# Performance work log

Hardware: AMD Instinct MI355X
Metric: run time of the kernel (lower is better)

The kernel has to match this reference:

```python
import jax, jax.numpy as jnp
import numpy as np

N_ATOMS = 50000
N_EDGES = 800000
NODE_DIM = 64
EDGE_DIM = 64
FULL_DIM = 2 * NODE_DIM + EDGE_DIM
BN_EPS = 1e-5


def setup_inputs() -> dict:
    key = jax.random.key(0)
    ks = jax.random.split(key, 8)
    atom_features = jax.random.normal(ks[0], (N_ATOMS, NODE_DIM), dtype=jnp.float32)
    edge_features = jax.random.normal(ks[1], (N_EDGES, EDGE_DIM), dtype=jnp.float32)
    edge_indices = jax.random.randint(ks[2], (N_EDGES, 2), 0, N_ATOMS, dtype=jnp.int64)
    lim = 1.0 / np.sqrt(FULL_DIM)
    W_filter = jax.random.uniform(ks[3], (NODE_DIM, FULL_DIM), jnp.float32, -lim, lim)
    b_filter = jax.random.uniform(ks[4], (NODE_DIM,), jnp.float32, -lim, lim)
    W_core = jax.random.uniform(ks[5], (NODE_DIM, FULL_DIM), jnp.float32, -lim, lim)
    b_core = jax.random.uniform(ks[6], (NODE_DIM,), jnp.float32, -lim, lim)
    gamma_filter = jnp.ones((NODE_DIM,), jnp.float32)
    beta_filter = jnp.zeros((NODE_DIM,), jnp.float32)
    gamma_core = jnp.ones((NODE_DIM,), jnp.float32)
    beta_core = jnp.zeros((NODE_DIM,), jnp.float32)
    return {
        "atom_features": atom_features,
        "edge_features": edge_features,
        "W_filter": W_filter, "b_filter": b_filter,
        "gamma_filter": gamma_filter, "beta_filter": beta_filter,
        "W_core": W_core, "b_core": b_core,
        "gamma_core": gamma_core, "beta_core": beta_core,
        "edge_indices": edge_indices,
    }


def _batchnorm(x, gamma, beta):
    # training-mode BN over the edge axis (biased variance, as torch uses for normalization)
    mean = jnp.mean(x, axis=0)
    var = jnp.mean(jnp.square(x - mean), axis=0)
    return (x - mean) * jax.lax.rsqrt(var + BN_EPS) * gamma + beta


def reference(atom_features, edge_features, W_filter, b_filter, gamma_filter,
              beta_filter, W_core, b_core, gamma_core, beta_core, edge_indices):
    src = edge_indices[:, 0]
    dst = edge_indices[:, 1]
    # z_ij: [E, 2*node_dim + edge_dim]
    z = jnp.concatenate([atom_features[dst], atom_features[src], edge_features], axis=1)
    signal = jax.nn.softplus(_batchnorm(z @ W_core.T + b_core, gamma_core, beta_core))
    gate = jax.nn.sigmoid(_batchnorm(z @ W_filter.T + b_filter, gamma_filter, beta_filter))
    message = gate * signal  # [E, node_dim]
    nbr_sumed = jax.ops.segment_sum(message, dst, num_segments=atom_features.shape[0])
    return atom_features + nbr_sumed
```

## Files before the change

### kernel.cpp

```cpp
#include <hip/hip_runtime.h>
#include <hip/hip_bf16.h>
#include <math.h>

#define N_ATOMS   50000
#define N_EDGES   800000
#define KDIM      192
#define BN_EPS    1e-5f

#define TILE_E     64
#define TPB        5
#define NTILES     (N_EDGES / TILE_E)
#define GRID1      (NTILES / TPB)
#define STAT_SLOTS 32
#define ZSTRIDE    200
#define NSCANBLK   ((N_ATOMS + 255) / 256)

typedef __attribute__((ext_vector_type(8))) __bf16 bf16x8;
typedef __attribute__((ext_vector_type(4))) float  f32x4;
typedef __attribute__((ext_vector_type(4))) unsigned short u16x4;

__device__ __forceinline__ ushort f2bf(float f) {
    union { float f; unsigned u; } v; v.f = f;
    unsigned u = v.u;
    return (ushort)((u + 0x7FFFu + ((u >> 16) & 1u)) >> 16);
}
__device__ __forceinline__ float bf2f(unsigned hi16) {
    union { unsigned u; float f; } v; v.u = hi16 << 16; return v.f;
}
__device__ __forceinline__ float msgf(unsigned pv, float sc_c, float sh_c,
                                      float sc_f, float sh_f) {
    float pc = fmaf(bf2f(pv & 0xFFFFu), sc_c, sh_c);
    float pf = fmaf(bf2f(pv >> 16),     sc_f, sh_f);
    float sp = fmaxf(pc, 0.f) + __logf(1.f + __expf(-fabsf(pc)));
    float sg = 1.f / (1.f + __expf(-pf));
    return sp * sg;
}

__device__ __forceinline__ void gather_issue(
    const float* __restrict__ atom, const float* __restrict__ edgef,
    const int* __restrict__ eidx, int tilebase, int tid, f32x4* v)
{
    const int er = tid >> 4, f4 = tid & 15;
#pragma unroll
    for (int it = 0; it < 12; ++it) {
        const int seg = it >> 2;
        const int e   = (it & 3) * 16 + er;
        const float* srcp;
        if (seg == 0)      srcp = atom  + (size_t)eidx[2 * (tilebase + e) + 1] * 64;
        else if (seg == 1) srcp = atom  + (size_t)eidx[2 * (tilebase + e)] * 64;
        else               srcp = edgef + (size_t)(tilebase + e) * 64;
        v[it] = *(const f32x4*)(srcp + f4 * 4);
    }
}

__device__ __forceinline__ void gather_commit(const f32x4* v, ushort* zl, int tid)
{
    const int er = tid >> 4, f4 = tid & 15;
#pragma unroll
    for (int it = 0; it < 12; ++it) {
        const int seg = it >> 2;
        const int e   = (it & 3) * 16 + er;
        u16x4 b;
        b.x = f2bf(v[it].x); b.y = f2bf(v[it].y);
        b.z = f2bf(v[it].z); b.w = f2bf(v[it].w);
        *(u16x4*)&zl[e * ZSTRIDE + seg * 64 + f4 * 4] = b;
    }
}

__global__ __launch_bounds__(256) void gemm_stats_store(
    const float* __restrict__ atom, const float* __restrict__ edgef,
    const ushort* __restrict__ Wb, const int* __restrict__ eidx,
    const unsigned* __restrict__ row_start, const unsigned* __restrict__ rank,
    float* __restrict__ stat_partial, unsigned* __restrict__ ws_pre,
    int do_store)
{
    __shared__ __align__(16) ushort zbuf[2][TILE_E * ZSTRIDE];
    __shared__ unsigned perml[TPB * TILE_E];
    const int tid  = threadIdx.x;
    const int lane = tid & 63, wave = tid >> 6;
    const int ch = wave >> 1, rp = wave & 1;
    const int row = lane & 15, quad = lane >> 4;

    const int t0 = blockIdx.x * TPB;
    if (do_store) {
        for (int i = tid; i < TPB * TILE_E; i += 256) {
            const int e = t0 * TILE_E + i;
            const int d = eidx[2 * e + 1];
            perml[i] = row_start[d] + rank[e];
        }
    }

    bf16x8 bfr[2][2][6];
#pragma unroll
    for (int m = 0; m < 2; ++m)
#pragma unroll
        for (int nt = 0; nt < 2; ++nt)
#pragma unroll
            for (int ks = 0; ks < 6; ++ks)
                bfr[m][nt][ks] = *(const bf16x8*)&Wb[
                    (size_t)(m * 64 + ch * 32 + nt * 16 + row) * KDIM + ks * 32 + quad * 8];

    float s[2][2] = {{0.f, 0.f}, {0.f, 0.f}};
    float q[2][2] = {{0.f, 0.f}, {0.f, 0.f}};

    f32x4 pre[12];
    gather_issue(atom, edgef, eidx, t0 * TILE_E, tid, pre);

    for (int tt = 0; tt < TPB; ++tt) {
        ushort* zl = zbuf[tt & 1];
        gather_commit(pre, zl, tid);
        __syncthreads();
        if (tt + 1 < TPB)
            gather_issue(atom, edgef, eidx, (t0 + tt + 1) * TILE_E, tid, pre);

#pragma unroll
        for (int ett = 0; ett < 2; ++ett) {
            const ushort* zb = zl + ((2 * rp + ett) * 16 + row) * ZSTRIDE;
            bf16x8 a[6];
#pragma unroll
            for (int ks = 0; ks < 6; ++ks)
                a[ks] = *(const bf16x8*)&zb[ks * 32 + quad * 8];
            f32x4 acc[2][2];
#pragma unroll
            for (int m = 0; m < 2; ++m)
#pragma unroll
                for (int nt = 0; nt < 2; ++nt)
                    acc[m][nt] = (f32x4){0.f, 0.f, 0.f, 0.f};
#pragma unroll
            for (int ks = 0; ks < 6; ++ks)
#pragma unroll
                for (int m = 0; m < 2; ++m)
#pragma unroll
                    for (int nt = 0; nt < 2; ++nt)
                        acc[m][nt] = __builtin_amdgcn_mfma_f32_16x16x32_bf16(
                            a[ks], bfr[m][nt][ks], acc[m][nt], 0, 0, 0);
#pragma unroll
            for (int nt = 0; nt < 2; ++nt) {
                const int c = ch * 32 + nt * 16 + row;
#pragma unroll
                for (int r = 0; r < 4; ++r) {
                    float vc = acc[0][nt][r], vf = acc[1][nt][r];
                    s[0][nt] += vc; q[0][nt] += vc * vc;
                    s[1][nt] += vf; q[1][nt] += vf * vf;
                    if (do_store) {
                        const int eloc = (2 * rp + ett) * 16 + quad * 4 + r;
                        const unsigned pos = perml[tt * TILE_E + eloc];
                        unsigned pack = (unsigned)f2bf(vc) | ((unsigned)f2bf(vf) << 16);
                        ws_pre[(size_t)pos * 64 + c] = pack;
                    }
                }
            }
        }
    }

    float* slot = stat_partial + (size_t)(blockIdx.x & (STAT_SLOTS - 1)) * 256;
#pragma unroll
    for (int m = 0; m < 2; ++m)
#pragma unroll
        for (int nt = 0; nt < 2; ++nt) {
            float sv = s[m][nt], qv = q[m][nt];
            sv += __shfl_xor(sv, 16, 64); sv += __shfl_xor(sv, 32, 64);
            qv += __shfl_xor(qv, 16, 64); qv += __shfl_xor(qv, 32, 64);
            if (lane < 16) {
                int c = ch * 32 + nt * 16 + lane;
                atomicAdd(slot + m * 128 + c, sv);
                atomicAdd(slot + m * 128 + 64 + c, qv);
            }
        }
}

__global__ __launch_bounds__(256) void setup_all(
    const float* __restrict__ Wc, const float* __restrict__ Wf,
    ushort* __restrict__ Wb, float* __restrict__ stat_partial,
    unsigned* __restrict__ counts)
{
    int i = blockIdx.x * 256 + threadIdx.x;
    if (i < 2 * 64 * KDIM) {
        float v = (i < 64 * KDIM) ? Wc[i] : Wf[i - 64 * KDIM];
        Wb[i] = f2bf(v);
    }
    if (i < STAT_SLOTS * 256) stat_partial[i] = 0.f;
    if (i < N_ATOMS) counts[i] = 0u;
}

__global__ void finalize_stats(const float* __restrict__ stat_partial,
                               const float* __restrict__ gc, const float* __restrict__ btc,
                               const float* __restrict__ gf, const float* __restrict__ btf,
                               float* __restrict__ params)
{
    int t = threadIdx.x;
    bool isf = t >= 64;
    int j = t & 63;
    float s = 0.f, q = 0.f;
    for (int slot = 0; slot < STAT_SLOTS; slot++) {
        const float* sp = stat_partial + (size_t)slot * 256 + (isf ? 128 : 0);
        s += sp[j];
        q += sp[64 + j];
    }
    float mean = s / (float)N_EDGES;
    float var  = q / (float)N_EDGES - mean * mean;
    float inv  = rsqrtf(var + BN_EPS);
    float gamma = isf ? gf[j] : gc[j];
    float beta  = isf ? btf[j] : btc[j];
    float scale = gamma * inv;
    float shift = beta - mean * scale;
    params[t]       = scale;
    params[128 + t] = shift;
}

__global__ __launch_bounds__(256) void hist_rank(const int* __restrict__ eidx,
                                                 unsigned* __restrict__ counts,
                                                 unsigned* __restrict__ rank)
{
    int e = blockIdx.x * 256 + threadIdx.x;
    rank[e] = atomicAdd(&counts[eidx[2 * e + 1]], 1u);
}

__global__ __launch_bounds__(256) void scan_a(const unsigned* __restrict__ counts,
                                              unsigned* __restrict__ row_start,
                                              unsigned* __restrict__ blksum)
{
    __shared__ unsigned sh[256];
    const int tid = threadIdx.x;
    const int i = blockIdx.x * 256 + tid;
    unsigned v = (i < N_ATOMS) ? counts[i] : 0u;
    sh[tid] = v;
    __syncthreads();
    for (int off = 1; off < 256; off <<= 1) {
        unsigned t = (tid >= off) ? sh[tid - off] : 0u;
        __syncthreads();
        sh[tid] += t;
        __syncthreads();
    }
    if (i < N_ATOMS) row_start[i] = sh[tid] - v;
    if (tid == 255) blksum[blockIdx.x] = sh[tid];
}

__global__ void scan_b(unsigned* __restrict__ blksum)
{
    __shared__ unsigned sh[256];
    const int tid = threadIdx.x;
    unsigned v = (tid < NSCANBLK) ? blksum[tid] : 0u;
    sh[tid] = v;
    __syncthreads();
    for (int off = 1; off < 256; off <<= 1) {
        unsigned t = (tid >= off) ? sh[tid - off] : 0u;
        __syncthreads();
        sh[tid] += t;
        __syncthreads();
    }
    if (tid < NSCANBLK) blksum[tid] = sh[tid] - v;
}

__global__ __launch_bounds__(256) void init_row(unsigned* __restrict__ row_start,
                                                const unsigned* __restrict__ blksum)
{
    int i = blockIdx.x * 256 + threadIdx.x;
    if (i < N_ATOMS) row_start[i] += blksum[i >> 8];
    if (i == 0) row_start[N_ATOMS] = N_EDGES;
}

__global__ __launch_bounds__(256) void bn_act_reduce(
    const unsigned* __restrict__ ws_pre, const unsigned* __restrict__ row_start,
    const float* __restrict__ atom, const float* __restrict__ params,
    float* __restrict__ out)
{
    const int lane = threadIdx.x & 63;
    const int a    = blockIdx.x * 4 + (threadIdx.x >> 6);

    const float sc_c = params[lane],      sh_c = params[128 + lane];
    const float sc_f = params[64 + lane], sh_f = params[192 + lane];

    const unsigned jb = row_start[a];
    const unsigned n  = row_start[a + 1] - jb;
    const unsigned* base = ws_pre + (size_t)jb * 64 + lane;

    float acc = 0.f;
    unsigned k = 0;
    for (; k + 8 <= n; k += 8) {
        unsigned p[8];
#pragma unroll
        for (int u = 0; u < 8; ++u) p[u] = base[(size_t)(k + u) * 64];
#pragma unroll
        for (int u = 0; u < 8; ++u) acc += msgf(p[u], sc_c, sh_c, sc_f, sh_f);
    }
    for (; k < n; ++k) acc += msgf(base[(size_t)k * 64], sc_c, sh_c, sc_f, sh_f);

    out[(size_t)a * 64 + lane] = atom[(size_t)a * 64 + lane] + acc;
}

__global__ __launch_bounds__(256) void copy_out(const f32x4* __restrict__ src,
                                                f32x4* __restrict__ dst)
{
    int i = blockIdx.x * blockDim.x + threadIdx.x;
    dst[i] = src[i];
}

__global__ __launch_bounds__(256) void apply_scatter_fb(
    const float* __restrict__ atom, const float* __restrict__ edgef,
    const ushort* __restrict__ Wb, const int* __restrict__ eidx,
    const float* __restrict__ params, float* __restrict__ out)
{
    __shared__ __align__(16) ushort zl[TILE_E * ZSTRIDE];
    const int tid  = threadIdx.x;
    const int lane = tid & 63, wave = tid >> 6;
    const int ch = wave >> 1, rp = wave & 1;
    const int row = lane & 15, quad = lane >> 4;

    bf16x8 bfr[2][2][6];
#pragma unroll
    for (int m = 0; m < 2; ++m)
#pragma unroll
        for (int nt = 0; nt < 2; ++nt)
#pragma unroll
            for (int ks = 0; ks < 6; ++ks)
                bfr[m][nt][ks] = *(const bf16x8*)&Wb[
                    (size_t)(m * 64 + ch * 32 + nt * 16 + row) * KDIM + ks * 32 + quad * 8];

    float scc[2], shc[2], scf[2], shf[2];
#pragma unroll
    for (int nt = 0; nt < 2; ++nt) {
        int c = ch * 32 + nt * 16 + row;
        scc[nt] = params[c];        shc[nt] = params[128 + c];
        scf[nt] = params[64 + c];   shf[nt] = params[192 + c];
    }

    const int t0 = blockIdx.x * TPB;
    for (int tt = 0; tt < TPB; ++tt) {
        const int tilebase = (t0 + tt) * TILE_E;
        f32x4 pre[12];
        gather_issue(atom, edgef, eidx, tilebase, tid, pre);
        __syncthreads();
        gather_commit(pre, zl, tid);
        __syncthreads();
#pragma unroll
        for (int ett = 0; ett < 2; ++ett) {
            const ushort* zb = zl + ((2 * rp + ett) * 16 + row) * ZSTRIDE;
            bf16x8 a[6];
#pragma unroll
            for (int ks = 0; ks < 6; ++ks)
                a[ks] = *(const bf16x8*)&zb[ks * 32 + quad * 8];
            f32x4 acc[2][2];
#pragma unroll
            for (int m = 0; m < 2; ++m)
#pragma unroll
                for (int nt = 0; nt < 2; ++nt)
                    acc[m][nt] = (f32x4){0.f, 0.f, 0.f, 0.f};
#pragma unroll
            for (int ks = 0; ks < 6; ++ks)
#pragma unroll
                for (int m = 0; m < 2; ++m)
#pragma unroll
                    for (int nt = 0; nt < 2; ++nt)
                        acc[m][nt] = __builtin_amdgcn_mfma_f32_16x16x32_bf16(
                            a[ks], bfr[m][nt][ks], acc[m][nt], 0, 0, 0);
#pragma unroll
            for (int nt = 0; nt < 2; ++nt) {
                int c = ch * 32 + nt * 16 + row;
#pragma unroll
                for (int r = 0; r < 4; ++r) {
                    float pc = fmaf(acc[0][nt][r], scc[nt], shc[nt]);
                    float pf = fmaf(acc[1][nt][r], scf[nt], shf[nt]);
                    float sp = fmaxf(pc, 0.f) + __logf(1.f + __expf(-fabsf(pc)));
                    float sg = 1.f / (1.f + __expf(-pf));
                    int eloc = (2 * rp + ett) * 16 + quad * 4 + r;
                    int d = eidx[2 * (tilebase + eloc) + 1];
                    atomicAdd(out + (size_t)d * 64 + c, sp * sg);
                }
            }
        }
    }
}

extern "C" void kernel_launch(void* const* d_in, const int* in_sizes, int n_in,
                              void* d_out, int out_size, void* d_ws, size_t ws_size,
                              hipStream_t stream)
{
    const float* atom  = (const float*)d_in[0];
    const float* edgef = (const float*)d_in[1];
    const float* Wf    = (const float*)d_in[2];
    const float* gf    = (const float*)d_in[4];
    const float* btf   = (const float*)d_in[5];
    const float* Wc    = (const float*)d_in[6];
    const float* gc    = (const float*)d_in[8];
    const float* btc   = (const float*)d_in[9];
    const int*   eidx  = (const int*)d_in[10];
    float* out = (float*)d_out;

    unsigned* ws_pre       = (unsigned*)d_ws;
    float*    stat_partial = (float*)(ws_pre + (size_t)N_EDGES * 64);
    float*    params       = stat_partial + STAT_SLOTS * 256;
    ushort*   Wb           = (ushort*)(params + 256);
    unsigned* counts       = (unsigned*)(Wb + 2 * 64 * KDIM);
    unsigned* row_start    = counts + N_ATOMS;
    unsigned* blksum       = row_start + N_ATOMS + 1;
    unsigned* rank         = blksum + 256;

    const size_t need_full = (size_t)((char*)(rank + N_EDGES) - (char*)d_ws);
    const int full = (ws_size >= need_full) ? 1 : 0;

    setup_all<<<256, 256, 0, stream>>>(Wc, Wf, Wb, stat_partial, counts);

    if (full) {
        hist_rank<<<N_EDGES / 256, 256, 0, stream>>>(eidx, counts, rank);
        scan_a<<<NSCANBLK, 256, 0, stream>>>(counts, row_start, blksum);
        scan_b<<<1, 256, 0, stream>>>(blksum);
        init_row<<<NSCANBLK, 256, 0, stream>>>(row_start, blksum);
        gemm_stats_store<<<GRID1, 256, 0, stream>>>(atom, edgef, Wb, eidx,
                                                    row_start, rank,
                                                    stat_partial, ws_pre, 1);
        finalize_stats<<<1, 128, 0, stream>>>(stat_partial, gc, btc, gf, btf, params);
        bn_act_reduce<<<N_ATOMS / 4, 256, 0, stream>>>(ws_pre, row_start,
                                                       atom, params, out);
    } else {
        gemm_stats_store<<<GRID1, 256, 0, stream>>>(atom, edgef, Wb, eidx,
                                                    (unsigned*)counts ,
                                                    (unsigned*)counts ,
                                                    stat_partial, ws_pre, 0);
        finalize_stats<<<1, 128, 0, stream>>>(stat_partial, gc, btc, gf, btf, params);
        copy_out<<<(N_ATOMS * 64 / 4) / 256, 256, 0, stream>>>(
            (const f32x4*)atom, (f32x4*)out);
        apply_scatter_fb<<<GRID1, 256, 0, stream>>>(atom, edgef, Wb, eidx,
                                                    params, out);
    }
}
```

Before: 493.7 us.

## Pre-convert atom features to bf16 for gathers and double tiles per block

Measured after the change: 482.1 us. -2.3%, faster.

```diff
diff --git a/kernel.cpp b/kernel.cpp
--- a/kernel.cpp
+++ b/kernel.cpp
@@ -8,7 +8,7 @@
 #define BN_EPS    1e-5f
 
 #define TILE_E     64
-#define TPB        5
+#define TPB        10
 #define NTILES     (N_EDGES / TILE_E)
 #define GRID1      (NTILES / TPB)
 #define STAT_SLOTS 32
@@ -34,6 +34,47 @@
     float sp = fmaxf(pc, 0.f) + __logf(1.f + __expf(-fabsf(pc)));
     float sg = 1.f / (1.f + __expf(-pf));
     return sp * sg;
+}
+
+__device__ __forceinline__ void gather_issue_m(
+    const ushort* __restrict__ atom_bf, const float* __restrict__ edgef,
+    const int* __restrict__ eidx, int tilebase, int tid,
+    u16x4* va, f32x4* ve)
+{
+    const int er = tid >> 4, f4 = tid & 15;
+#pragma unroll
+    for (int it = 0; it < 8; ++it) {
+        const int seg = it >> 2;
+        const int e   = (it & 3) * 16 + er;
+        const ushort* srcp =
+            atom_bf + (size_t)eidx[2 * (tilebase + e) + (seg == 0 ? 1 : 0)] * 64;
+        va[it] = *(const u16x4*)(srcp + f4 * 4);
+    }
+#pragma unroll
+    for (int it = 0; it < 4; ++it) {
+        const int e = it * 16 + er;
+        ve[it] = *(const f32x4*)(edgef + (size_t)(tilebase + e) * 64 + f4 * 4);
+    }
+}
+
+__device__ __forceinline__ void gather_commit_m(
+    const u16x4* va, const f32x4* ve, ushort* zl, int tid)
+{
+    const int er = tid >> 4, f4 = tid & 15;
+#pragma unroll
+    for (int it = 0; it < 8; ++it) {
+        const int seg = it >> 2;
+        const int e   = (it & 3) * 16 + er;
+        *(u16x4*)&zl[e * ZSTRIDE + seg * 64 + f4 * 4] = va[it];
+    }
+#pragma unroll
+    for (int it = 0; it < 4; ++it) {
+        const int e = it * 16 + er;
+        u16x4 b;
+        b.x = f2bf(ve[it].x); b.y = f2bf(ve[it].y);
+        b.z = f2bf(ve[it].z); b.w = f2bf(ve[it].w);
+        *(u16x4*)&zl[e * ZSTRIDE + 128 + f4 * 4] = b;
+    }
 }
 
 __device__ __forceinline__ void gather_issue(
@@ -68,7 +109,7 @@
 }
 
 __global__ __launch_bounds__(256) void gemm_stats_store(
-    const float* __restrict__ atom, const float* __restrict__ edgef,
+    const ushort* __restrict__ atom_bf, const float* __restrict__ edgef,
     const ushort* __restrict__ Wb, const int* __restrict__ eidx,
     const unsigned* __restrict__ row_start, const unsigned* __restrict__ rank,
     float* __restrict__ stat_partial, unsigned* __restrict__ ws_pre,
@@ -103,15 +144,17 @@
     float s[2][2] = {{0.f, 0.f}, {0.f, 0.f}};
     float q[2][2] = {{0.f, 0.f}, {0.f, 0.f}};
 
-    f32x4 pre[12];
-    gather_issue(atom, edgef, eidx, t0 * TILE_E, tid, pre);
+    u16x4 pva[8];
+    f32x4 pve[4];
+    gather_issue_m(atom_bf, edgef, eidx, t0 * TILE_E, tid, pva, pve);
 
     for (int tt = 0; tt < TPB; ++tt) {
         ushort* zl = zbuf[tt & 1];
-        gather_commit(pre, zl, tid);
+        gather_commit_m(pva, pve, zl, tid);
         __syncthreads();
         if (tt + 1 < TPB)
-            gather_issue(atom, edgef, eidx, (t0 + tt + 1) * TILE_E, tid, pre);
+            gather_issue_m(atom_bf, edgef, eidx, (t0 + tt + 1) * TILE_E, tid,
+                           pva, pve);
 
 #pragma unroll
         for (int ett = 0; ett < 2; ++ett) {
@@ -171,8 +214,9 @@
 
 __global__ __launch_bounds__(256) void setup_all(
     const float* __restrict__ Wc, const float* __restrict__ Wf,
-    ushort* __restrict__ Wb, float* __restrict__ stat_partial,
-    unsigned* __restrict__ counts)
+    const float* __restrict__ atom,
+    ushort* __restrict__ Wb, ushort* __restrict__ atom_bf,
+    float* __restrict__ stat_partial, unsigned* __restrict__ counts)
 {
     int i = blockIdx.x * 256 + threadIdx.x;
     if (i < 2 * 64 * KDIM) {
@@ -181,6 +225,12 @@
     }
     if (i < STAT_SLOTS * 256) stat_partial[i] = 0.f;
     if (i < N_ATOMS) counts[i] = 0u;
+    for (int j = i; j < N_ATOMS * 64 / 4; j += 256 * 256) {
+        f32x4 v = ((const f32x4*)atom)[j];
+        u16x4 b;
+        b.x = f2bf(v.x); b.y = f2bf(v.y); b.z = f2bf(v.z); b.w = f2bf(v.w);
+        ((u16x4*)atom_bf)[j] = b;
+    }
 }
 
 __global__ void finalize_stats(const float* __restrict__ stat_partial,
@@ -213,7 +263,8 @@
                                                  unsigned* __restrict__ rank)
 {
     int e = blockIdx.x * 256 + threadIdx.x;
-    rank[e] = atomicAdd(&counts[eidx[2 * e + 1]], 1u);
+    int2 p = ((const int2*)eidx)[e];
+    rank[e] = atomicAdd(&counts[p.y], 1u);
 }
 
 __global__ __launch_bounds__(256) void scan_a(const unsigned* __restrict__ counts,
@@ -296,10 +347,23 @@
     dst[i] = src[i];
 }
 
-__global__ __launch_bounds__(256) void apply_scatter_fb(
+__global__ __launch_bounds__(256) void convert_weights_fb(
+    const float* __restrict__ Wc, const float* __restrict__ Wf,
+    ushort* __restrict__ Wb, float* __restrict__ stat_partial)
+{
+    int i = blockIdx.x * 256 + threadIdx.x;
+    if (i < 2 * 64 * KDIM) {
+        float v = (i < 64 * KDIM) ? Wc[i] : Wf[i - 64 * KDIM];
+        Wb[i] = f2bf(v);
+    }
+    if (i < STAT_SLOTS * 256) stat_partial[i] = 0.f;
+}
+
+#define TPB_FB 5
+__global__ __launch_bounds__(256) void gemm_stats_fb(
     const float* __restrict__ atom, const float* __restrict__ edgef,
     const ushort* __restrict__ Wb, const int* __restrict__ eidx,
-    const float* __restrict__ params, float* __restrict__ out)
+    float* __restrict__ stat_partial)
 {
     __shared__ __align__(16) ushort zl[TILE_E * ZSTRIDE];
     const int tid  = threadIdx.x;
@@ -317,6 +381,87 @@
                 bfr[m][nt][ks] = *(const bf16x8*)&Wb[
                     (size_t)(m * 64 + ch * 32 + nt * 16 + row) * KDIM + ks * 32 + quad * 8];
 
+    float s[2][2] = {{0.f, 0.f}, {0.f, 0.f}};
+    float q[2][2] = {{0.f, 0.f}, {0.f, 0.f}};
+
+    const int t0 = blockIdx.x * TPB_FB;
+    for (int tt = 0; tt < TPB_FB; ++tt) {
+        const int tilebase = (t0 + tt) * TILE_E;
+        f32x4 pre[12];
+        gather_issue(atom, edgef, eidx, tilebase, tid, pre);
+        __syncthreads();
+        gather_commit(pre, zl, tid);
+        __syncthreads();
+#pragma unroll
+        for (int ett = 0; ett < 2; ++ett) {
+            const ushort* zb = zl + ((2 * rp + ett) * 16 + row) * ZSTRIDE;
+            bf16x8 a[6];
+#pragma unroll
+            for (int ks = 0; ks < 6; ++ks)
+                a[ks] = *(const bf16x8*)&zb[ks * 32 + quad * 8];
+            f32x4 acc[2][2];
+#pragma unroll
+            for (int m = 0; m < 2; ++m)
+#pragma unroll
+                for (int nt = 0; nt < 2; ++nt)
+                    acc[m][nt] = (f32x4){0.f, 0.f, 0.f, 0.f};
+#pragma unroll
+            for (int ks = 0; ks < 6; ++ks)
+#pragma unroll
+                for (int m = 0; m < 2; ++m)
+#pragma unroll
+                    for (int nt = 0; nt < 2; ++nt)
+                        acc[m][nt] = __builtin_amdgcn_mfma_f32_16x16x32_bf16(
+                            a[ks], bfr[m][nt][ks], acc[m][nt], 0, 0, 0);
+#pragma unroll
+            for (int nt = 0; nt < 2; ++nt) {
+#pragma unroll
+                for (int r = 0; r < 4; ++r) {
+                    float vc = acc[0][nt][r], vf = acc[1][nt][r];
+                    s[0][nt] += vc; q[0][nt] += vc * vc;
+                    s[1][nt] += vf; q[1][nt] += vf * vf;
+                }
+            }
+        }
+    }
+
+    float* slot = stat_partial + (size_t)(blockIdx.x & (STAT_SLOTS - 1)) * 256;
+#pragma unroll
+    for (int m = 0; m < 2; ++m)
+#pragma unroll
+        for (int nt = 0; nt < 2; ++nt) {
+            float sv = s[m][nt], qv = q[m][nt];
+            sv += __shfl_xor(sv, 16, 64); sv += __shfl_xor(sv, 32, 64);
+            qv += __shfl_xor(qv, 16, 64); qv += __shfl_xor(qv, 32, 64);
+            if (lane < 16) {
+                int c = ch * 32 + nt * 16 + lane;
+                atomicAdd(slot + m * 128 + c, sv);
+                atomicAdd(slot + m * 128 + 64 + c, qv);
+            }
+        }
+}
+
+__global__ __launch_bounds__(256) void apply_scatter_fb(
+    const float* __restrict__ atom, const float* __restrict__ edgef,
+    const ushort* __restrict__ Wb, const int* __restrict__ eidx,
+    const float* __restrict__ params, float* __restrict__ out)
+{
+    __shared__ __align__(16) ushort zl[TILE_E * ZSTRIDE];
+    const int tid  = threadIdx.x;
+    const int lane = tid & 63, wave = tid >> 6;
+    const int ch = wave >> 1, rp = wave & 1;
+    const int row = lane & 15, quad = lane >> 4;
+
+    bf16x8 bfr[2][2][6];
+#pragma unroll
+    for (int m = 0; m < 2; ++m)
+#pragma unroll
+        for (int nt = 0; nt < 2; ++nt)
+#pragma unroll
+            for (int ks = 0; ks < 6; ++ks)
+                bfr[m][nt][ks] = *(const bf16x8*)&Wb[
+                    (size_t)(m * 64 + ch * 32 + nt * 16 + row) * KDIM + ks * 32 + quad * 8];
+
     float scc[2], shc[2], scf[2], shf[2];
 #pragma unroll
     for (int nt = 0; nt < 2; ++nt) {
@@ -325,8 +470,8 @@
         scf[nt] = params[64 + c];   shf[nt] = params[192 + c];
     }
 
-    const int t0 = blockIdx.x * TPB;
-    for (int tt = 0; tt < TPB; ++tt) {
+    const int t0 = blockIdx.x * TPB_FB;
+    for (int tt = 0; tt < TPB_FB; ++tt) {
         const int tilebase = (t0 + tt) * TILE_E;
         f32x4 pre[12];
         gather_issue(atom, edgef, eidx, tilebase, tid, pre);
@@ -393,34 +538,34 @@
     ushort*   Wb           = (ushort*)(params + 256);
     unsigned* counts       = (unsigned*)(Wb + 2 * 64 * KDIM);
     unsigned* row_start    = counts + N_ATOMS;
-    unsigned* blksum       = row_start + N_ATOMS + 1;
-    unsigned* rank         = blksum + 256;
-
-    const size_t need_full = (size_t)((char*)(rank + N_EDGES) - (char*)d_ws);
+    unsigned* rank         = row_start + N_ATOMS + 2;
+    ushort*   atom_bf      = (ushort*)(rank + N_EDGES);
+    unsigned* blksum       = (unsigned*)(atom_bf + (size_t)N_ATOMS * 64);
+
+    const size_t need_full = (size_t)((char*)(blksum + 256) - (char*)d_ws);
     const int full = (ws_size >= need_full) ? 1 : 0;
 
-    setup_all<<<256, 256, 0, stream>>>(Wc, Wf, Wb, stat_partial, counts);
-
     if (full) {
+        setup_all<<<256, 256, 0, stream>>>(Wc, Wf, atom, Wb, atom_bf,
+                                           stat_partial, counts);
         hist_rank<<<N_EDGES / 256, 256, 0, stream>>>(eidx, counts, rank);
         scan_a<<<NSCANBLK, 256, 0, stream>>>(counts, row_start, blksum);
         scan_b<<<1, 256, 0, stream>>>(blksum);
         init_row<<<NSCANBLK, 256, 0, stream>>>(row_start, blksum);
-        gemm_stats_store<<<GRID1, 256, 0, stream>>>(atom, edgef, Wb, eidx,
+        gemm_stats_store<<<GRID1, 256, 0, stream>>>(atom_bf, edgef, Wb, eidx,
                                                     row_start, rank,
                                                     stat_partial, ws_pre, 1);
         finalize_stats<<<1, 128, 0, stream>>>(stat_partial, gc, btc, gf, btf, params);
         bn_act_reduce<<<N_ATOMS / 4, 256, 0, stream>>>(ws_pre, row_start,
                                                        atom, params, out);
     } else {
-        gemm_stats_store<<<GRID1, 256, 0, stream>>>(atom, edgef, Wb, eidx,
-                                                    (unsigned*)counts ,
-                                                    (unsigned*)counts ,
-                                                    stat_partial, ws_pre, 0);
+        convert_weights_fb<<<256, 256, 0, stream>>>(Wc, Wf, Wb, stat_partial);
+        gemm_stats_fb<<<NTILES / TPB_FB, 256, 0, stream>>>(atom, edgef, Wb, eidx,
+                                                           stat_partial);
         finalize_stats<<<1, 128, 0, stream>>>(stat_partial, gc, btc, gf, btf, params);
         copy_out<<<(N_ATOMS * 64 / 4) / 256, 256, 0, stream>>>(
             (const f32x4*)atom, (f32x4*)out);
-        apply_scatter_fb<<<GRID1, 256, 0, stream>>>(atom, edgef, Wb, eidx,
-                                                    params, out);
-    }
-}
+        apply_scatter_fb<<<NTILES / TPB_FB, 256, 0, stream>>>(atom, edgef, Wb, eidx,
+                                                              params, out);
+    }
+}
```
